# Kernel optimization log

Hardware: AMD Instinct MI355X
Metric: run time of the kernel (lower is better)

The kernel has to match this reference:

```python
import jax, jax.numpy as jnp
from jax import lax
import numpy as np

SR = 48000; FRAME = 960; NFFT = 3840; NWIN = 1024; NFREQ = NFFT // 2 + 1
B = 8; LF = 200; C_CONT = 192; C_SPK = 256; C_INT = 512; NL = 6; MLP = 3; KS = 7


def _interp_linear(x, Lout):
    # F.interpolate(mode='linear', align_corners=False) on (B,C,Lin)
    Lin = x.shape[-1]
    pos = (jnp.arange(Lout, dtype=jnp.float32) + 0.5) * (Lin / Lout) - 0.5
    pos = jnp.clip(pos, 0.0, Lin - 1.0)
    i0 = jnp.floor(pos).astype(jnp.int32)
    i1 = jnp.minimum(i0 + 1, Lin - 1)
    w = pos - i0.astype(jnp.float32)
    return x[..., i0] * (1.0 - w) + x[..., i1] * w


def _interp_nearest(x, Lout):
    Lin = x.shape[-1]
    idx = jnp.floor(jnp.arange(Lout, dtype=jnp.float32) * (Lin / Lout)).astype(jnp.int32)
    return x[..., idx]


def _ln(x, g, b, eps=1e-5):
    # channel-wise LayerNorm on (B,C,L)
    m = jnp.mean(x, axis=1, keepdims=True)
    v = jnp.var(x, axis=1, keepdims=True)
    return (x - m) * lax.rsqrt(v + eps) * g[None, :, None] + b[None, :, None]


def _dwconv(x, w):  # x (B,C,L), w (C,K), zero pad 'same'
    C = x.shape[1]; K = w.shape[-1]
    return lax.conv_general_dilated(x, w[:, None, :], (1,), ((K // 2, K // 2),),
                                    feature_group_count=C,
                                    dimension_numbers=('NCH', 'OIH', 'NCH'))


def _convnext(x, dw_w, dw_b, ln, pw1_w, pw1_b, pw2_w, pw2_b):
    for i in range(dw_w.shape[0]):  # fixed small layer count
        h = _dwconv(x, dw_w[i]) + dw_b[i][None, :, None]
        h = _ln(h, ln[i, 0], ln[i, 1])
        h = jnp.einsum('oc,bcl->bol', pw1_w[i], h) + pw1_b[i][None, :, None]
        h = jax.nn.gelu(h, approximate=False)
        h = jnp.einsum('oc,bcl->bol', pw2_w[i], h) + pw2_b[i][None, :, None]
        x = x + h
    return x


def _forward(content, f0, energy, spk,
             s_in_w, s_in_b, s_in_norm, s_dw_w, s_dw_b, s_ln, s_pw1_w, s_pw1_b,
             s_pw2_w, s_pw2_b, s_out_norm, s_amp_w, s_amp_b, s_ker_w, s_ker_b,
             f_in_w, f_in_b, f_dw_w, f_dw_b, f_ln, f_pw1_w, f_pw1_b,
             f_pw2_w, f_pw2_b, f_out_norm, f_out_w, f_out_b):
    Bc, _, Lf = content.shape
    Lw = Lf * FRAME
    # fused input projection: 4 parallel 1x1 convs == one matmul over concat
    xin = jnp.concatenate([content,
                           jnp.broadcast_to(spk, (Bc, spk.shape[1], Lf)),
                           jnp.log(jax.nn.relu(f0) + 1e-6),
                           energy], axis=1)  # (B,450,Lf)

    # ---------- FirSourceNet trunk ----------
    x = jnp.einsum('oc,bcl->bol', s_in_w, xin) + s_in_b[None, :, None]
    x = _ln(x, s_in_norm[0], s_in_norm[1])
    x = _convnext(x, s_dw_w, s_dw_b, s_ln, s_pw1_w, s_pw1_b, s_pw2_w, s_pw2_b)
    x = _ln(x, s_out_norm[0], s_out_norm[1])
    amps = jax.nn.elu(jnp.einsum('oc,bcl->bol', s_amp_w, x) + s_amp_b[None, :, None]) + 1.0
    kernels = jax.nn.elu(jnp.einsum('oc,bcl->bol', s_ker_w, x) + s_ker_b[None, :, None]) + 1.0  # (B,1921,Lf)

    # ---------- harmonic oscillator (Dirichlet kernel of all harmonics) ----------
    fs = _interp_linear(f0, Lw)                                   # (B,1,Lw)
    uv = _interp_nearest((f0 > 20.0).astype(jnp.float32), Lw)
    pix = jnp.cumsum(jnp.pi * fs / SR, axis=2) % jnp.pi
    a = jnp.round(SR / jnp.maximum(fs, 20.0) * 0.5) * 2.0 + 1.0
    harm = jnp.where(pix < 1e-8, 1.0, jnp.sin(a * pix) / (a * jnp.sin(pix))) * uv
    harm = harm * _interp_linear(amps, Lw)

    # ---------- filtered noise via STFT shaping (hop=FRAME, hann) ----------
    noise = jax.random.uniform(jax.random.key(123), (Bc, Lw), dtype=jnp.float32)
    win = 0.5 - 0.5 * jnp.cos(2.0 * jnp.pi * jnp.arange(NFFT, dtype=jnp.float32) / NFFT)
    pad = NFFT // 2
    xp = jnp.pad(noise, ((0, 0), (pad, pad)), mode='reflect')
    idx = (jnp.arange(Lf + 1) * FRAME)[:, None] + jnp.arange(NFFT)[None, :]
    spec = jnp.fft.rfft(xp[:, idx] * win, axis=-1).transpose(0, 2, 1)      # (B,NFREQ,Lf+1)
    spec = jnp.pad(spec[:, :, 1:] * kernels, ((0, 0), (0, 0), (1, 0)))     # drop 1st frame, shape back
    ft = jnp.fft.irfft(spec.transpose(0, 2, 1), n=NFFT, axis=-1) * win     # (B,Lf+1,NFFT)
    Lpad = NFFT + Lf * FRAME
    y = jnp.zeros((Bc, Lpad), jnp.float32).at[:, idx].add(ft)
    wn = jnp.zeros((Lpad,), jnp.float32).at[idx.reshape(-1)].add(jnp.tile(win * win, Lf + 1))
    y = y / jnp.where(wn > 1e-11, wn, 1.0)
    dsp = harm[:, 0, :] + y[:, pad:pad + Lw]                               # (B,Lw) harmonic+noise source

    # ---------- FirFilterNet: time-varying framed FIR ----------
    x = jnp.einsum('oc,bcl->bol', f_in_w, xin) + f_in_b[None, :, None]
    x = _convnext(x, f_dw_w, f_dw_b, f_ln, f_pw1_w, f_pw1_b, f_pw2_w, f_pw2_b)
    x = _ln(x, f_out_norm[0], f_out_norm[1])
    xe = jnp.pad(x, ((0, 0), (0, 0), (3, 3)), mode='edge')                 # replicate pad
    filt = lax.conv_general_dilated(xe, f_out_w, (1,), 'VALID',
                                    dimension_numbers=('NCH', 'OIH', 'NCH')) + f_out_b[None, :, None]
    filt = filt.transpose(0, 2, 1)                                         # (B,Lf,NWIN)
    # per-frame correlation: grouped conv with B*Lf groups
    src = jnp.pad(dsp.reshape(Bc, Lf, FRAME), ((0, 0), (0, 0), (NWIN, NWIN - 1)))  # (B,Lf,3007)
    out = lax.conv_general_dilated(src.reshape(1, Bc * Lf, FRAME + 2 * NWIN - 1),
                                   filt.reshape(Bc * Lf, 1, NWIN), (1,), 'VALID',
                                   feature_group_count=Bc * Lf,
                                   dimension_numbers=('NCH', 'OIH', 'NCH'))
    out = out.reshape(Bc, Lf, FRAME + NWIN)                                # (B,Lf,1984)
    # fold: overlap-add frames at stride FRAME
    idx2 = (jnp.arange(Lf) * FRAME)[:, None] + jnp.arange(FRAME + NWIN)[None, :]
    folded = jnp.zeros((Bc, Lw + NWIN), jnp.float32).at[:, idx2].add(out)
    return folded[:, None, :Lw]                                            # (B,1,Lw)


def setup_inputs() -> dict:
    key = jax.random.key(0)
    ks = iter(jax.random.split(key, 64))
    def nrm(shape, fan):
        return jax.random.normal(next(ks), shape, dtype=jnp.float32) * (fan ** -0.5)
    d = {}
    d['content'] = jax.random.normal(next(ks), (B, C_CONT, LF), dtype=jnp.float32)
    d['f0'] = jax.random.uniform(next(ks), (B, 1, LF), minval=80.0, maxval=480.0)
    d['energy'] = jax.random.uniform(next(ks), (B, 1, LF), dtype=jnp.float32)
    d['spk'] = jax.random.normal(next(ks), (B, C_SPK, 1), dtype=jnp.float32)
    CIN = C_CONT + C_SPK + 2
    HID = C_INT * MLP
    ones = jnp.ones((C_INT,), jnp.float32); zeros = jnp.zeros((C_INT,), jnp.float32)
    norm2 = jnp.stack([ones, zeros])
    normL = jnp.broadcast_to(norm2, (NL, 2, C_INT)) + 0.0
    for p in ('s', 'f'):
        d[p + '_in_w'] = nrm((C_INT, CIN), CIN); d[p + '_in_b'] = jnp.zeros((C_INT,), jnp.float32)
        d[p + '_dw_w'] = nrm((NL, C_INT, KS), KS); d[p + '_dw_b'] = jnp.zeros((NL, C_INT), jnp.float32)
        d[p + '_ln'] = normL
        d[p + '_pw1_w'] = nrm((NL, HID, C_INT), C_INT); d[p + '_pw1_b'] = jnp.zeros((NL, HID), jnp.float32)
        d[p + '_pw2_w'] = nrm((NL, C_INT, HID), HID); d[p + '_pw2_b'] = jnp.zeros((NL, C_INT), jnp.float32)
        d[p + '_out_norm'] = norm2
    d['s_in_norm'] = norm2
    d['s_amp_w'] = nrm((1, C_INT), C_INT); d['s_amp_b'] = jnp.zeros((1,), jnp.float32)
    d['s_ker_w'] = nrm((NFREQ, C_INT), C_INT); d['s_ker_b'] = jnp.zeros((NFREQ,), jnp.float32)
    d['f_out_w'] = nrm((NWIN, C_INT, KS), C_INT * KS); d['f_out_b'] = jnp.zeros((NWIN,), jnp.float32)
    return d


def reference(content, f0, energy, spk,
              s_in_w, s_in_b, s_in_norm, s_dw_w, s_dw_b, s_ln, s_pw1_w, s_pw1_b,
              s_pw2_w, s_pw2_b, s_out_norm, s_amp_w, s_amp_b, s_ker_w, s_ker_b,
              f_in_w, f_in_b, f_dw_w, f_dw_b, f_ln, f_pw1_w, f_pw1_b,
              f_pw2_w, f_pw2_b, f_out_norm, f_out_w, f_out_b):
    return _forward(content, f0, energy, spk,
                    s_in_w, s_in_b, s_in_norm, s_dw_w, s_dw_b, s_ln, s_pw1_w, s_pw1_b,
                    s_pw2_w, s_pw2_b, s_out_norm, s_amp_w, s_amp_b, s_ker_w, s_ker_b,
                    f_in_w, f_in_b, f_dw_w, f_dw_b, f_ln, f_pw1_w, f_pw1_b,
                    f_pw2_w, f_pw2_b, f_out_norm, f_out_w, f_out_b)
```

## Files before the change

kernel.cpp:

```cpp
#include <hip/hip_runtime.h>
#include <hip/hip_bf16.h>
#include <math.h>
#include <stdint.h>

#define FRAME 960
#define NFFT  3840
#define NWIN  1024
#define NFREQ 1921
#define NB    8
#define LF    200
#define LW    192000
#define CIN   450
#define CI    512
#define HID   1536
#define NL    6
#define NCH   188
#define NK2   3842
#define MTOT  1600
#define MB2   3200
#define SWID  3968
#define MPAD  1664

typedef __attribute__((ext_vector_type(8))) short short8v;
typedef __attribute__((ext_vector_type(4))) float f32x4;
typedef __attribute__((address_space(3))) uint32_t lds_u32;
typedef const __attribute__((address_space(1))) uint32_t glb_u32;

__device__ __forceinline__ uint32_t rotl32(uint32_t v, int r) { return (v << r) | (v >> (32 - r)); }
__device__ __forceinline__ void threefry2x32(uint32_t k0, uint32_t k1, uint32_t& x0, uint32_t& x1) {
  uint32_t ks2 = k0 ^ k1 ^ 0x1BD11BDAu;
  x0 += k0; x1 += k1;
#define TFR(r) { x0 += x1; x1 = rotl32(x1, r); x1 ^= x0; }
  TFR(13) TFR(15) TFR(26) TFR(6)  x0 += k1;  x1 += ks2 + 1u;
  TFR(17) TFR(29) TFR(16) TFR(24) x0 += ks2; x1 += k0 + 2u;
  TFR(13) TFR(15) TFR(26) TFR(6)  x0 += k0;  x1 += k1 + 3u;
  TFR(17) TFR(29) TFR(16) TFR(24) x0 += k1;  x1 += ks2 + 4u;
  TFR(13) TFR(15) TFR(26) TFR(6)  x0 += ks2; x1 += k0 + 5u;
#undef TFR
}
__device__ __forceinline__ float noiseval(int b, int m) {
  if (m < 0) m = -m;
  if (m >= LW) m = 2 * LW - 2 - m;
  uint32_t x0 = 0u, x1 = (uint32_t)(b * LW + m);
  threefry2x32(0u, 123u, x0, x1);
  uint32_t bits = x0 ^ x1;
  return __uint_as_float((bits >> 9) | 0x3f800000u) - 1.0f;
}
__device__ __forceinline__ float winf(int j) {
  return 0.5f - 0.5f * cosf((6.283185307179586f * (float)j) / 3840.0f);
}
__device__ __forceinline__ unsigned short f2bf(float v) {
  uint32_t b = __float_as_uint(v);
  return (unsigned short)((b + 0x7FFFu + ((b >> 16) & 1u)) >> 16);
}
__device__ __forceinline__ float bf2f(unsigned short h) {
  return __uint_as_float(((uint32_t)h) << 16);
}
__device__ __forceinline__ uint32_t pack2(float a, float b, bool lo) {
  unsigned short ha = f2bf(a), hb = f2bf(b);
  if (!lo) return (uint32_t)ha | ((uint32_t)hb << 16);
  return (uint32_t)f2bf(a - bf2f(ha)) | ((uint32_t)f2bf(b - bf2f(hb)) << 16);
}
__device__ __forceinline__ int xcd_remap(int lin, int nwg) {
  int q = nwg >> 3, r = nwg & 7;
  int xcd = lin & 7, base = lin >> 3;
  int start = (xcd < r) ? xcd * (q + 1) : r * (q + 1) + (xcd - r) * q;
  return start + base;
}

__global__ void ctab_fill(float* __restrict__ ct) {
  int j = blockIdx.x * 256 + threadIdx.x;
  if (j < NFFT) ct[j] = cosf((6.283185307179586f * (float)j) / 3840.0f);
}

__global__ void build_xin_pk(const float* __restrict__ content, const float* __restrict__ f0,
                             const float* __restrict__ energy, const float* __restrict__ spk,
                             uint32_t* __restrict__ PH) {
  int idx = blockIdx.x * 256 + threadIdx.x;
  if (idx >= MB2 * 240) return;
  int row = idx / 240, cp = idx % 240;
  int rb = row % MTOT;
  int b = rb / LF, l = rb % LF;
  float v2[2];
#pragma unroll
  for (int u = 0; u < 2; ++u) {
    int c = cp * 2 + u;
    float v = 0.f;
    if (c < 192)       v = content[((size_t)b * 192 + c) * LF + l];
    else if (c < 448)  v = spk[b * 256 + (c - 192)];
    else if (c == 448) v = logf(fmaxf(f0[b * LF + l], 0.0f) + 1e-6f);
    else if (c == 449) v = energy[b * LF + l];
    v2[u] = v;
  }
  PH[idx] = pack2(v2[0], v2[1], false);
}

__global__ void pack_w(const float* __restrict__ W, uint32_t* __restrict__ PH,
                       int M, int K, int Kp2, int total) {
  int idx = blockIdx.x * 256 + threadIdx.x;
  if (idx >= total) return;
  int m = idx / Kp2, kp = idx % Kp2;
  int k = kp * 2;
  float v0 = (m < M && k < K) ? W[(size_t)m * K + k] : 0.f;
  float v1 = (m < M && (k + 1) < K) ? W[(size_t)m * K + k + 1] : 0.f;
  PH[idx] = pack2(v0, v1, false);
}

__global__ void pack_w2(const float* __restrict__ Ws, const float* __restrict__ Wf,
                        uint32_t* __restrict__ PH, int M, int K, int Kp2, int total) {
  int idx = blockIdx.x * 256 + threadIdx.x;
  if (idx >= 2 * total) return;
  int half = idx >= total;
  const float* W = half ? Wf : Ws;
  int t = idx - half * total;
  int m = t / Kp2, kp = t % Kp2;
  int k = kp * 2;
  float v0 = (m < M && k < K) ? W[(size_t)m * K + k] : 0.f;
  float v1 = (m < M && (k + 1) < K) ? W[(size_t)m * K + k + 1] : 0.f;
  PH[idx] = pack2(v0, v1, false);
}

__global__ void pack_wN(const float* __restrict__ Ws, const float* __restrict__ Wf, size_t lstride,
                        uint32_t* __restrict__ PH, int M, int K, int Kp2, int perset, int total) {
  int idx = blockIdx.x * 256 + threadIdx.x;
  if (idx >= total) return;
  int l = idx / (2 * perset);
  int r = idx - l * 2 * perset;
  int half = r >= perset;
  const float* W = (half ? Wf : Ws) + (size_t)l * lstride;
  int t = r - half * perset;
  int m = t / Kp2, kp = t % Kp2;
  int k = kp * 2;
  float v0 = (m < M && k < K) ? W[(size_t)m * K + k] : 0.f;
  float v1 = (m < M && (k + 1) < K) ? W[(size_t)m * K + k + 1] : 0.f;
  PH[idx] = pack2(v0, v1, false);
}

__global__ __launch_bounds__(256) void gemm_bf(
    const uint16_t* __restrict__ WH, const uint16_t* __restrict__ XH,
    const float* __restrict__ bias, const float* __restrict__ bias2,
    const float* __restrict__ res,
    float* __restrict__ outF, uint16_t* __restrict__ outH,
    int M, int Kp, int mtiles, int ntiles, int mode, int act, int nsp, size_t woff)
{
  __shared__ __align__(16) char smem[2][2][4096];
  int nwg = mtiles * ntiles;
  int wg = xcd_remap(blockIdx.x, nwg);
  int mtile = wg / ntiles, ntile = wg % ntiles;
  int m0 = mtile * 64, n0 = ntile * 64;
  int tid = threadIdx.x;
  int lane = tid & 63, w = tid >> 6;
  int wm = w >> 1, wn = w & 1;
  int rowg = Kp >> 3;
  int phases = Kp >> 5;

  int opsel = w >> 1, whalf = w & 1;
  const uint16_t* gb = (opsel == 0) ? WH : XH;
  if (opsel == 0 && ntile >= nsp) gb += woff;
  int row0 = (opsel == 0) ? m0 : n0;
  f32x4 acc[2][2];
#pragma unroll
  for (int i = 0; i < 2; ++i)
#pragma unroll
    for (int j = 0; j < 2; ++j) acc[i][j] = (f32x4){0.f, 0.f, 0.f, 0.f};

  auto stage = [&](int buf, int p) {
    int kg0 = p * 4;
#pragma unroll
    for (int c = 0; c < 2; ++c) {
      int i = whalf * 2 + c;
      int r = i * 16 + (lane >> 2);
      int scg = lane & 3;
      int sgsel = scg ^ (((lane >> 2) >> 1) & 3);
      const uint16_t* src = gb + (size_t)(row0 + r) * rowg * 8 + (size_t)(kg0 + sgsel) * 8;
      __builtin_amdgcn_global_load_lds((glb_u32*)src, (lds_u32*)(&smem[buf][opsel][0] + i * 1024), 16, 0, 0);
    }
  };

  stage(0, 0);
  __syncthreads();
  int fr = lane & 15, fg = lane >> 4;
  int fsw = ((fr >> 1) & 3);
  int aoff0 = (wm * 32 + fr) * 64 + (fg ^ fsw) * 16;
  int aoff1 = (wm * 32 + 16 + fr) * 64 + (fg ^ fsw) * 16;
  int boff0 = (wn * 32 + fr) * 64 + (fg ^ fsw) * 16;
  int boff1 = (wn * 32 + 16 + fr) * 64 + (fg ^ fsw) * 16;

  for (int p = 0; p < phases; ++p) {
    int cur = p & 1;
    if (p + 1 < phases) stage(cur ^ 1, p + 1);
    short8v ah0 = *(const short8v*)(&smem[cur][0][0] + aoff0);
    short8v ah1 = *(const short8v*)(&smem[cur][0][0] + aoff1);
    short8v bh0 = *(const short8v*)(&smem[cur][1][0] + boff0);
    short8v bh1 = *(const short8v*)(&smem[cur][1][0] + boff1);
    acc[0][0] = __builtin_amdgcn_mfma_f32_16x16x32_bf16(ah0, bh0, acc[0][0], 0, 0, 0);
    acc[0][1] = __builtin_amdgcn_mfma_f32_16x16x32_bf16(ah0, bh1, acc[0][1], 0, 0, 0);
    acc[1][0] = __builtin_amdgcn_mfma_f32_16x16x32_bf16(ah1, bh0, acc[1][0], 0, 0, 0);
    acc[1][1] = __builtin_amdgcn_mfma_f32_16x16x32_bf16(ah1, bh1, acc[1][1], 0, 0, 0);
    __syncthreads();
  }

#pragma unroll
  for (int mi = 0; mi < 2; ++mi)
#pragma unroll
    for (int ni = 0; ni < 2; ++ni)
#pragma unroll
      for (int r = 0; r < 4; ++r) {
        int m = m0 + wm * 32 + mi * 16 + ((lane >> 4) << 2) + r;
        int n = n0 + wn * 32 + ni * 16 + (lane & 15);
        if (m >= M) continue;
        float v = acc[mi][ni][r];
        if (bias) v += (bias2 && n >= nsp * 64) ? bias2[m] : bias[m];
        if (act == 1)      v = 0.5f * v * (1.0f + erff(v * 0.7071067811865475f));
        else if (act == 2) v = (v > 0.f ? v : expm1f(v)) + 1.0f;
        if (mode == 0) {
          if (res) v += res[(size_t)n * M + m];
          outF[(size_t)n * M + m] = v;
        } else if (mode == 1) {
          outH[(size_t)n * M + m] = f2bf(v);
        } else {
          outH[(size_t)n * NFREQ + m] = f2bf(v);
        }
      }
}

__global__ __launch_bounds__(256) void gemm_fwd128(
    const uint16_t* __restrict__ AH, const uint16_t* __restrict__ TH,
    const uint16_t* __restrict__ KERH, uint16_t* __restrict__ SH)
{
  __shared__ __align__(16) char smem[2][12288];
  int wg = xcd_remap(blockIdx.x, 62 * 13);
  int ntile = wg / 13, mtile = wg % 13;
  int m0 = mtile * 128, n0 = ntile * 64;
  int tid = threadIdx.x;
  int lane = tid & 63, w = tid >> 6;
  int wm = w >> 1, wn = w & 1;
  f32x4 acc[4][2];
#pragma unroll
  for (int i = 0; i < 4; ++i)
#pragma unroll
    for (int j = 0; j < 2; ++j) acc[i][j] = (f32x4){0.f, 0.f, 0.f, 0.f};

  auto stage = [&](int buf, int p) {
    if (w < 2) {
#pragma unroll
      for (int i = 0; i < 4; ++i) {
        int ci = w * 4 + i;
        int gl = ci * 64 + lane;
        int row = gl >> 2, cg = gl & 3;
        int sg = cg ^ ((row >> 1) & 3);
        const uint16_t* src = AH + (size_t)(m0 + row) * 3840 + p * 32 + sg * 8;
        __builtin_amdgcn_global_load_lds((glb_u32*)src, (lds_u32*)(&smem[buf][0] + ci * 1024), 16, 0, 0);
      }
    } else {
#pragma unroll
      for (int i = 0; i < 2; ++i) {
        int ci = (w - 2) * 2 + i;
        int gl = ci * 64 + lane;
        int row = gl >> 2, cg = gl & 3;
        int sg = cg ^ ((row >> 1) & 3);
        const uint16_t* src = TH + (size_t)(n0 + row) * 3840 + p * 32 + sg * 8;
        __builtin_amdgcn_global_load_lds((glb_u32*)src, (lds_u32*)(&smem[buf][8192] + ci * 1024), 16, 0, 0);
      }
    }
  };

  stage(0, 0);
  __syncthreads();
  int fr = lane & 15, fg = lane >> 4;

  for (int p = 0; p < 120; ++p) {
    int cur = p & 1;
    if (p + 1 < 120) stage(cur ^ 1, p + 1);
    short8v a_h[4], b_h[2];
#pragma unroll
    for (int q = 0; q < 4; ++q) {
      int ra = wm * 64 + q * 16 + fr;
      a_h[q] = *(const short8v*)(&smem[cur][0] + ra * 64 + ((fg ^ ((ra >> 1) & 3)) << 4));
    }
#pragma unroll
    for (int s = 0; s < 2; ++s) {
      int rb = wn * 32 + s * 16 + fr;
      b_h[s] = *(const short8v*)(&smem[cur][8192] + rb * 64 + ((fg ^ ((rb >> 1) & 3)) << 4));
    }
#pragma unroll
    for (int mi = 0; mi < 4; ++mi)
#pragma unroll
      for (int ni = 0; ni < 2; ++ni)
        acc[mi][ni] = __builtin_amdgcn_mfma_f32_16x16x32_bf16(a_h[mi], b_h[ni], acc[mi][ni], 0, 0, 0);
    __syncthreads();
  }

#pragma unroll
  for (int mi = 0; mi < 4; ++mi)
#pragma unroll
    for (int ni = 0; ni < 2; ++ni)
#pragma unroll
      for (int r = 0; r < 4; ++r) {
        int m = m0 + wm * 64 + mi * 16 + ((lane >> 4) << 2) + r;
        int n = n0 + wn * 32 + ni * 16 + (lane & 15);
        if (m < MTOT) {
          float o = 0.f;
          if (n < NK2) {
            int k = n >> 1;
            float kv = bf2f(KERH[(size_t)m * NFREQ + k]);
            bool edge = (k == 0) || (k == 1920);
            float mult = edge ? (1.0f / NFFT) : (2.0f / NFFT);
            o = acc[mi][ni][r] * kv * mult;
            if ((n & 1) && edge) o = 0.f;
          }
          SH[(size_t)m * SWID + n] = f2bf(o);
        }
      }
}

__global__ void twfill_v(const float* __restrict__ ct, uint32_t* __restrict__ VH) {
  int idx = blockIdx.x * 256 + threadIdx.x;
  if (idx >= NFFT * (SWID / 2)) return;
  int j = idx / (SWID / 2), kp = idx % (SWID / 2);
  float v2[2] = {0.f, 0.f};
#pragma unroll
  for (int u = 0; u < 2; ++u) {
    int k2 = kp * 2 + u;
    if (k2 < NK2) {
      int k = k2 >> 1;
      int m = (j * k) % NFFT;
      m += (k2 & 1) * 960;
      if (m >= NFFT) m -= NFFT;
      v2[u] = ct[m];
    }
  }
  VH[idx] = pack2(v2[0], v2[1], false);
}

__global__ __launch_bounds__(256) void gemm_invNT(
    const uint16_t* __restrict__ SH, const uint16_t* __restrict__ VH,
    const float* __restrict__ ct, float* __restrict__ ft)
{
  __shared__ __align__(16) char smem[2][12288];
  int wg = xcd_remap(blockIdx.x, 60 * 13);
  int ntile = wg / 13, mtile = wg % 13;
  int m0 = mtile * 128, n0 = ntile * 64;
  int tid = threadIdx.x;
  int lane = tid & 63, w = tid >> 6;
  int wm = w >> 1, wn = w & 1;
  f32x4 acc[4][2];
#pragma unroll
  for (int i = 0; i < 4; ++i)
#pragma unroll
    for (int j = 0; j < 2; ++j) acc[i][j] = (f32x4){0.f, 0.f, 0.f, 0.f};

  auto stage = [&](int buf, int p) {
    if (w < 2) {
#pragma unroll
      for (int i = 0; i < 4; ++i) {
        int ci = w * 4 + i;
        int gl = ci * 64 + lane;
        int row = gl >> 2, cg = gl & 3;
        int sg = cg ^ ((row >> 1) & 3);
        const uint16_t* src = SH + (size_t)(m0 + row) * SWID + p * 32 + sg * 8;
        __builtin_amdgcn_global_load_lds((glb_u32*)src, (lds_u32*)(&smem[buf][0] + ci * 1024), 16, 0, 0);
      }
    } else {
#pragma unroll
      for (int i = 0; i < 2; ++i) {
        int ci = (w - 2) * 2 + i;
        int gl = ci * 64 + lane;
        int row = gl >> 2, cg = gl & 3;
        int sg = cg ^ ((row >> 1) & 3);
        const uint16_t* src = VH + (size_t)(n0 + row) * SWID + p * 32 + sg * 8;
        __builtin_amdgcn_global_load_lds((glb_u32*)src, (lds_u32*)(&smem[buf][8192] + ci * 1024), 16, 0, 0);
      }
    }
  };

  stage(0, 0);
  __syncthreads();
  int fr = lane & 15, fg = lane >> 4;

  for (int p = 0; p < 124; ++p) {
    int cur = p & 1;
    if (p + 1 < 124) stage(cur ^ 1, p + 1);
    short8v a_h[4], b_h[2];
#pragma unroll
    for (int q = 0; q < 4; ++q) {
      int ra = wm * 64 + q * 16 + fr;
      a_h[q] = *(const short8v*)(&smem[cur][0] + ra * 64 + ((fg ^ ((ra >> 1) & 3)) << 4));
    }
#pragma unroll
    for (int s = 0; s < 2; ++s) {
      int rb = wn * 32 + s * 16 + fr;
      b_h[s] = *(const short8v*)(&smem[cur][8192] + rb * 64 + ((fg ^ ((rb >> 1) & 3)) << 4));
    }
#pragma unroll
    for (int mi = 0; mi < 4; ++mi)
#pragma unroll
      for (int ni = 0; ni < 2; ++ni)
        acc[mi][ni] = __builtin_amdgcn_mfma_f32_16x16x32_bf16(a_h[mi], b_h[ni], acc[mi][ni], 0, 0, 0);
    __syncthreads();
  }

#pragma unroll
  for (int mi = 0; mi < 4; ++mi)
#pragma unroll
    for (int ni = 0; ni < 2; ++ni)
#pragma unroll
      for (int r = 0; r < 4; ++r) {
        int m = m0 + wm * 64 + mi * 16 + ((lane >> 4) << 2) + r;
        int n = n0 + wn * 32 + ni * 16 + (lane & 15);
        if (m < MTOT) ft[(size_t)m * NFFT + n] = acc[mi][ni][r] * (0.5f - 0.5f * ct[n]);
      }
}

__global__ __launch_bounds__(256) void ln2_kernel(float* __restrict__ x, const float* __restrict__ g,
                                                  const float* __restrict__ bta,
                                                  uint32_t* __restrict__ PH) {
  int row = blockIdx.x * 4 + (threadIdx.x >> 6);
  int lane = threadIdx.x & 63;
  float* xr = x + (size_t)row * CI;
  int c0 = lane * 8;
  float4 v0 = *(float4*)&xr[c0], v1 = *(float4*)&xr[c0 + 4];
  float s = v0.x + v0.y + v0.z + v0.w + v1.x + v1.y + v1.z + v1.w;
#pragma unroll
  for (int m = 1; m < 64; m <<= 1) s += __shfl_xor(s, m, 64);
  float mean = s * (1.0f / CI);
  float d[8] = {v0.x - mean, v0.y - mean, v0.z - mean, v0.w - mean,
                v1.x - mean, v1.y - mean, v1.z - mean, v1.w - mean};
  float s2 = 0.f;
#pragma unroll
  for (int q = 0; q < 8; ++q) s2 += d[q] * d[q];
#pragma unroll
  for (int m = 1; m < 64; m <<= 1) s2 += __shfl_xor(s2, m, 64);
  float rs = rsqrtf(s2 * (1.0f / CI) + 1e-5f);
  float o[8];
#pragma unroll
  for (int q = 0; q < 8; ++q) o[q] = d[q] * rs * g[c0 + q] + bta[c0 + q];
  float4 w0 = {o[0], o[1], o[2], o[3]}, w1 = {o[4], o[5], o[6], o[7]};
  *(float4*)&xr[c0] = w0; *(float4*)&xr[c0 + 4] = w1;
  if (PH) {
    int base = (row * CI + c0) >> 1;
#pragma unroll
    for (int q = 0; q < 4; ++q)
      PH[base + q] = pack2(o[2 * q], o[2 * q + 1], false);
  }
}

__global__ __launch_bounds__(256) void dwln_kernel(const float* __restrict__ xs,
    const float* __restrict__ dws, const float* __restrict__ dbs,
    const float* __restrict__ gs, const float* __restrict__ bts,
    const float* __restrict__ dwf, const float* __restrict__ dbf,
    const float* __restrict__ gf, const float* __restrict__ btf,
    uint32_t* __restrict__ PH) {
  int row = blockIdx.x;
  int half = row >= MTOT;
  const float* dw = half ? dwf : dws;
  const float* db = half ? dbf : dbs;
  const float* g  = half ? gf : gs;
  const float* bt = half ? btf : bts;
  int rb = row - half * MTOT;
  int b = rb / LF, l = rb % LF;
  int rbase = half * MTOT + b * LF;
  int c = threadIdx.x * 2;
  float ax = db[c], ay = db[c + 1];
#pragma unroll
  for (int tau = 0; tau < 7; ++tau) {
    int j = l + tau - 3;
    if (j < 0 || j >= LF) continue;
    float2 xv = *(const float2*)&xs[((size_t)(rbase + j)) * CI + c];
    ax = fmaf(xv.x, dw[c * 7 + tau], ax);
    ay = fmaf(xv.y, dw[(c + 1) * 7 + tau], ay);
  }
  __shared__ float red[4], red2[4];
  float s = ax + ay;
#pragma unroll
  for (int m = 1; m < 64; m <<= 1) s += __shfl_xor(s, m, 64);
  if ((threadIdx.x & 63) == 0) red[threadIdx.x >> 6] = s;
  __syncthreads();
  float mean = (red[0] + red[1] + red[2] + red[3]) * (1.0f / CI);
  float dx = ax - mean, dy = ay - mean;
  float s2 = dx * dx + dy * dy;
#pragma unroll
  for (int m = 1; m < 64; m <<= 1) s2 += __shfl_xor(s2, m, 64);
  if ((threadIdx.x & 63) == 0) red2[threadIdx.x >> 6] = s2;
  __syncthreads();
  float var = (red2[0] + red2[1] + red2[2] + red2[3]) * (1.0f / CI);
  float rs = rsqrtf(var + 1e-5f);
  float vx = dx * rs * g[c] + bt[c];
  float vy = dy * rs * g[c + 1] + bt[c + 1];
  PH[(size_t)row * 256 + threadIdx.x] = pack2(vx, vy, false);
}

__global__ __launch_bounds__(256) void amps2_kernel(const float* __restrict__ x, const float* __restrict__ w,
                                                    const float* __restrict__ bias, float* __restrict__ amps) {
  int row = blockIdx.x * 4 + (threadIdx.x >> 6);
  int lane = threadIdx.x & 63;
  const float* xr = x + (size_t)row * CI;
  int c0 = lane * 8;
  float4 v0 = *(const float4*)&xr[c0], v1 = *(const float4*)&xr[c0 + 4];
  float4 w0 = *(const float4*)&w[c0], w1 = *(const float4*)&w[c0 + 4];
  float s = v0.x * w0.x + v0.y * w0.y + v0.z * w0.z + v0.w * w0.w
          + v1.x * w1.x + v1.y * w1.y + v1.z * w1.z + v1.w * w1.w;
#pragma unroll
  for (int m = 1; m < 64; m <<= 1) s += __shfl_xor(s, m, 64);
  if (lane == 0) {
    float a = s + bias[0];
    amps[row] = (a > 0.f ? a : expm1f(a)) + 1.0f;
  }
}

__global__ void im2col_pk(const float* __restrict__ x, uint32_t* __restrict__ PH) {
  int idx = blockIdx.x * 256 + threadIdx.x;
  if (idx >= MTOT * 1792) return;
  int row = idx / 1792, kp = idx % 1792;
  int b = row / LF, l = row % LF;
  float v2[2];
#pragma unroll
  for (int u = 0; u < 2; ++u) {
    int kap = kp * 2 + u;
    int ch = kap / 7, tau = kap % 7;
    int j = l + tau - 3;
    j = j < 0 ? 0 : (j > LF - 1 ? LF - 1 : j);
    v2[u] = x[((size_t)b * LF + j) * CI + ch];
  }
  PH[idx] = pack2(v2[0], v2[1], false);
}

__global__ void pack_noise(const float* __restrict__ ct, uint32_t* __restrict__ AH) {
  int idx = blockIdx.x * 256 + threadIdx.x;
  if (idx >= MPAD * 1920) return;
  int t = idx / 1920, jp = idx % 1920;
  float v0 = 0.f, v1 = 0.f;
  if (t < MTOT) {
    int b = t / LF, tt = t % LF;
    int j = jp * 2;
    v0 = noiseval(b, tt * 960 + j - 960) * (0.5f - 0.5f * ct[j]);
    v1 = noiseval(b, tt * 960 + j - 959) * (0.5f - 0.5f * ct[j + 1]);
  }
  AH[idx] = pack2(v0, v1, false);
}

__global__ void twfill_pk(const float* __restrict__ ct, uint32_t* __restrict__ TH) {
  int idx = blockIdx.x * 256 + threadIdx.x;
  if (idx >= SWID * 1920) return;
  int k2 = idx / 1920, jp = idx % 1920;
  float v2[2] = {0.f, 0.f};
  if (k2 < NK2) {
    int k = k2 >> 1;
    int add = (k2 & 1) * 960;
#pragma unroll
    for (int u = 0; u < 2; ++u) {
      int j = jp * 2 + u;
      int m = (j * k) % NFFT;
      m += add;
      if (m >= NFFT) m -= NFFT;
      v2[u] = ct[m];
    }
  }
  TH[idx] = pack2(v2[0], v2[1], false);
}

__global__ __launch_bounds__(256) void cumsum1(const float* __restrict__ f0, float* __restrict__ fs,
                                               double* __restrict__ csum) {
  int b = blockIdx.y, ch = blockIdx.x;
  int base = ch * 1024;
  double s = 0.0;
  for (int q = 0; q < 4; ++q) {
    int n = base + threadIdx.x * 4 + q;
    if (n < LW) {
      float pos = ((float)n + 0.5f) * (200.0f / 192000.0f) - 0.5f;
      pos = fminf(fmaxf(pos, 0.0f), 199.0f);
      int i0 = (int)pos;
      int i1 = min(i0 + 1, 199);
      float w = pos - (float)i0;
      float fsv = f0[b * LF + i0] * (1.0f - w) + f0[b * LF + i1] * w;
      fs[(size_t)b * LW + n] = fsv;
      s += (double)((3.14159274101257324f * fsv) / 48000.0f);
    }
  }
  __shared__ double sh[256];
  sh[threadIdx.x] = s;
  __syncthreads();
  for (int o2 = 128; o2 > 0; o2 >>= 1) {
    if (threadIdx.x < o2) sh[threadIdx.x] += sh[threadIdx.x + o2];
    __syncthreads();
  }
  if (threadIdx.x == 0) csum[b * NCH + ch] = sh[0];
}

__global__ __launch_bounds__(256) void harm_kernel(
    const float* __restrict__ fs, const double* __restrict__ csum,
    const float* __restrict__ f0, const float* __restrict__ amps,
    float* __restrict__ harm) {
  int b = blockIdx.y, ch = blockIdx.x;
  const float* fsb = fs + (size_t)b * LW;
  int base = ch * 1024;
  int tid = threadIdx.x;
  double p[4]; double s = 0.0;
  int n0 = base + tid * 4;
  for (int q = 0; q < 4; ++q) {
    int n = n0 + q; float sm = 0.f;
    if (n < LW) sm = (3.14159274101257324f * fsb[n]) / 48000.0f;
    s += (double)sm; p[q] = s;
  }
  __shared__ double sh[256];
  sh[tid] = (tid < ch) ? csum[b * NCH + tid] : 0.0;
  __syncthreads();
  for (int o2 = 128; o2 > 0; o2 >>= 1) {
    if (tid < o2) sh[tid] += sh[tid + o2];
    __syncthreads();
  }
  double cbase = sh[0];
  __syncthreads();
  sh[tid] = s; __syncthreads();
  for (int o2 = 1; o2 < 256; o2 <<= 1) {
    double v = (tid >= o2) ? sh[tid - o2] : 0.0;
    __syncthreads();
    sh[tid] += v;
    __syncthreads();
  }
  double excl = cbase + (tid > 0 ? sh[tid - 1] : 0.0);
  const double PID = (double)3.14159274101257324f;
  for (int q = 0; q < 4; ++q) {
    int n = n0 + q; if (n >= LW) break;
    double S = excl + p[q];
    float pixf = (float)fmod(S, PID);
    float fsv = fsb[n];
    float a = rintf(48000.0f / fmaxf(fsv, 20.0f) * 0.5f) * 2.0f + 1.0f;
    float D = (pixf < 1e-8f) ? 1.0f : (sinf(a * pixf) / (a * sinf(pixf)));
    int ui = n / 960;
    float uv = (f0[b * LF + ui] > 20.0f) ? 1.0f : 0.0f;
    float posA = ((float)n + 0.5f) * (200.0f / 192000.0f) - 0.5f;
    posA = fminf(fmaxf(posA, 0.0f), 199.0f);
    int i0 = (int)posA;
    int i1 = min(i0 + 1, 199);
    float w = posA - (float)i0;
    float ampI = amps[b * LF + i0] * (1.0f - w) + amps[b * LF + i1] * w;
    harm[(size_t)b * LW + n] = (D * uv) * ampI;
  }
}

__global__ __launch_bounds__(256) void fir5_kernel(const float* __restrict__ ft,
                                                   const float* __restrict__ harm,
                                                   const float* __restrict__ filt,
                                                   const float* __restrict__ ct,
                                                   float* __restrict__ outf) {
  int t = blockIdx.x, b = blockIdx.y;
  __shared__ float frp[3456];
  __shared__ float fl[NWIN];
  int tid = threadIdx.x;
  for (int i = tid; i < 3456; i += 256) frp[i] = 0.f;
  __syncthreads();
  for (int i = tid; i < FRAME; i += 256) {
    int n = t * FRAME + i;
    int p = n + 1920;
    int t0 = (p > 3839) ? ((p - 2880) / 960) : 0;
    int t1 = p / FRAME; if (t1 > 200) t1 = 200;
    float y = 0.f, wn = 0.f;
    for (int tt = t0; tt <= t1; ++tt) {
      int j = p - FRAME * tt;
      float w = 0.5f - 0.5f * ct[j];
      wn += w * w;
      if (tt >= 1) y += ft[((size_t)b * LF + (tt - 1)) * NFFT + j];
    }
    float den = wn > 1e-11f ? wn : 1.0f;
    float dspv = harm[(size_t)b * LW + n] + y / den;
    int x = 1024 + i;
    frp[x + (x >> 3)] = dspv;
  }
  for (int i = tid; i < NWIN; i += 256) fl[i] = filt[((size_t)b * LF + t) * NWIN + i];
  __syncthreads();
  float a[8] = {0.f, 0.f, 0.f, 0.f, 0.f, 0.f, 0.f, 0.f};
  float wbuf[8];
  int base = 9 * tid;
#pragma unroll
  for (int r = 0; r < 8; ++r) wbuf[r] = frp[base + r];
  int nbase = base + 9;
  for (int tau8 = 0; tau8 < 128; ++tau8) {
    int nb = nbase + tau8 * 9;
#pragma unroll
    for (int r = 0; r < 8; ++r) {
      float fv = fl[tau8 * 8 + r];
#pragma unroll
      for (int q = 0; q < 8; ++q)
        a[q] = fmaf(wbuf[(r + q) & 7], fv, a[q]);
      wbuf[r] = frp[nb + r];
    }
  }
#pragma unroll
  for (int q = 0; q < 8; ++q) {
    int i = tid * 8 + q;
    if (i < 1984) outf[((size_t)b * LF + t) * 1984 + i] = a[q];
  }
}

__global__ void fold_kernel(const float* __restrict__ outf, float* __restrict__ out) {
  int idx = blockIdx.x * 256 + threadIdx.x;
  if (idx >= NB * LW) return;
  int b = idx / LW, n = idx % LW;
  int t0 = (n >= 1984) ? ((n - 1024) / 960) : 0;
  int t1 = n / 960; if (t1 > 199) t1 = 199;
  float acc = 0.f;
  for (int t = t0; t <= t1; ++t)
    acc += outf[((size_t)b * LF + t) * 1984 + (n - 960 * t)];
  out[idx] = acc;
}

extern "C" void kernel_launch(void* const* d_in, const int* in_sizes, int n_in,
                              void* d_out, int out_size, void* d_ws, size_t ws_size,
                              hipStream_t stream) {
  const float* content    = (const float*)d_in[0];
  const float* f0         = (const float*)d_in[1];
  const float* energy     = (const float*)d_in[2];
  const float* spk        = (const float*)d_in[3];
  const float* s_in_w     = (const float*)d_in[4];
  const float* s_in_b     = (const float*)d_in[5];
  const float* s_dw_w     = (const float*)d_in[6];
  const float* s_dw_b     = (const float*)d_in[7];
  const float* s_ln       = (const float*)d_in[8];
  const float* s_pw1_w    = (const float*)d_in[9];
  const float* s_pw1_b    = (const float*)d_in[10];
  const float* s_pw2_w    = (const float*)d_in[11];
  const float* s_pw2_b    = (const float*)d_in[12];
  const float* s_out_norm = (const float*)d_in[13];
  const float* f_in_w     = (const float*)d_in[14];
  const float* f_in_b     = (const float*)d_in[15];
  const float* f_dw_w     = (const float*)d_in[16];
  const float* f_dw_b     = (const float*)d_in[17];
  const float* f_ln       = (const float*)d_in[18];
  const float* f_pw1_w    = (const float*)d_in[19];
  const float* f_pw1_b    = (const float*)d_in[20];
  const float* f_pw2_w    = (const float*)d_in[21];
  const float* f_pw2_b    = (const float*)d_in[22];
  const float* f_out_norm = (const float*)d_in[23];
  const float* s_in_norm  = (const float*)d_in[24];
  const float* s_amp_w    = (const float*)d_in[25];
  const float* s_amp_b    = (const float*)d_in[26];
  const float* s_ker_w    = (const float*)d_in[27];
  const float* s_ker_b    = (const float*)d_in[28];
  const float* f_out_w    = (const float*)d_in[29];
  const float* f_out_b    = (const float*)d_in[30];

  char* W0 = (char*)d_ws;
  double*   CSUM  = (double*)W0;
  uint32_t* XINPH = (uint32_t*)(W0 + 12032);
  float*    XS    = (float*)   (W0 + 6156032);
  uint32_t* TPH   = (uint32_t*)(W0 + 12709632);
  uint16_t* KERH  = (uint16_t*)(W0 + 19263232);
  float*    AMPS  = (float*)   (W0 + 25410432);
  float*    FILT  = (float*)   (W0 + 25418624);
  float*    HARM  = (float*)   (W0 + 31972224);
  char*     R2    = W0 + 38116224;
  char*     FTR   = W0 + 64527232;
  char*     U     = W0 + 89103232;
  uint32_t* TH32  = (uint32_t*)(W0 + 114662272);
  float*    CTAB  = (float*)   (W0 + 175610752);
  uint32_t* XSPH = TPH;
  uint32_t* H15PH = (uint32_t*)R2;
  uint32_t* IMPH = (uint32_t*)R2;
  uint16_t* SH   = (uint16_t*)R2;
  float*    OUTF = (float*)R2;
  float*    FS   = (float*)FTR;
  float*    FT   = (float*)FTR;
  uint32_t* PW1PH_A = (uint32_t*)FTR;
  uint32_t* PW1PH_B = (uint32_t*)U;
  uint32_t* PW2PH = TH32;
  uint32_t* WINPH = (uint32_t*)R2;
  uint32_t* WPH  = (uint32_t*)U;
  uint16_t* AH   = (uint16_t*)U;

  (void)in_sizes; (void)n_in; (void)out_size; (void)ws_size;

  ctab_fill<<<dim3(15), 256, 0, stream>>>(CTAB);
  build_xin_pk<<<dim3((MB2 * 240 + 255) / 256), 256, 0, stream>>>(content, f0, energy, spk, XINPH);

  {
    int perset = HID * 256;
    int tot3 = 3 * 2 * perset;
    pack_wN<<<dim3((tot3 + 255) / 256), 256, 0, stream>>>(s_pw1_w, f_pw1_w, (size_t)HID * CI,
        PW1PH_A, HID, CI, 256, perset, tot3);
    pack_wN<<<dim3((tot3 + 255) / 256), 256, 0, stream>>>(s_pw1_w + (size_t)3 * HID * CI,
        f_pw1_w + (size_t)3 * HID * CI, (size_t)HID * CI,
        PW1PH_B, HID, CI, 256, perset, tot3);
    int tot6 = 6 * 2 * perset;
    pack_wN<<<dim3((tot6 + 255) / 256), 256, 0, stream>>>(s_pw2_w, f_pw2_w, (size_t)CI * HID,
        PW2PH, CI, HID, 768, perset, tot6);
  }
  {
    int total = CI * 240;
    pack_w2<<<dim3((2 * total + 255) / 256), 256, 0, stream>>>(s_in_w, f_in_w, WINPH, CI, CIN, 240, total);
  }

  gemm_bf<<<dim3(8 * 50), 256, 0, stream>>>((uint16_t*)WINPH, (uint16_t*)XINPH,
      s_in_b, f_in_b, nullptr, XS, nullptr, CI, 480, 8, 50, 0, 0, 25, (size_t)512 * 480);
  ln2_kernel<<<dim3(MTOT / 4), 256, 0, stream>>>(XS, s_in_norm, s_in_norm + CI, nullptr);
  for (int i = 0; i < NL; ++i) {
    dwln_kernel<<<dim3(MB2), 256, 0, stream>>>(XS,
        s_dw_w + (size_t)i * CI * 7, s_dw_b + (size_t)i * CI,
        s_ln + (size_t)(i * 2) * CI, s_ln + (size_t)(i * 2 + 1) * CI,
        f_dw_w + (size_t)i * CI * 7, f_dw_b + (size_t)i * CI,
        f_ln + (size_t)(i * 2) * CI, f_ln + (size_t)(i * 2 + 1) * CI,
        TPH);
    const uint16_t* w1h = (i < 3) ? (const uint16_t*)((char*)PW1PH_A + (size_t)i * 3145728)
                                  : (const uint16_t*)((char*)PW1PH_B + (size_t)(i - 3) * 3145728);
    gemm_bf<<<dim3(24 * 50), 256, 0, stream>>>(w1h, (uint16_t*)TPH,
        s_pw1_b + (size_t)i * HID, f_pw1_b + (size_t)i * HID, nullptr,
        nullptr, (uint16_t*)H15PH, HID, 512, 24, 50, 1, 1, 25, (size_t)1536 * 512);
    const uint16_t* w2h = (const uint16_t*)((char*)PW2PH + (size_t)i * 3145728);
    gemm_bf<<<dim3(8 * 50), 256, 0, stream>>>(w2h, (uint16_t*)H15PH,
        s_pw2_b + (size_t)i * CI, f_pw2_b + (size_t)i * CI, XS,
        XS, nullptr, CI, 1536, 8, 50, 0, 0, 25, (size_t)512 * 1536);
  }

  ln2_kernel<<<dim3(MTOT / 4), 256, 0, stream>>>(XS, s_out_norm, s_out_norm + CI, XSPH);
  amps2_kernel<<<dim3(MTOT / 4), 256, 0, stream>>>(XS, s_amp_w, s_amp_b, AMPS);
  {
    int total = 1984 * 256;
    pack_w<<<dim3((total + 255) / 256), 256, 0, stream>>>(s_ker_w, WPH, NFREQ, CI, 256, total);
  }
  gemm_bf<<<dim3(31 * 25), 256, 0, stream>>>((uint16_t*)WPH, (uint16_t*)XSPH,
      s_ker_b, nullptr, nullptr, nullptr, KERH, NFREQ, 512, 31, 25, 2, 2, 1000, 0);

  ln2_kernel<<<dim3(MTOT / 4), 256, 0, stream>>>(XS + (size_t)MTOT * CI, f_out_norm, f_out_norm + CI, nullptr);
  im2col_pk<<<dim3((MTOT * 1792 + 255) / 256), 256, 0, stream>>>(XS + (size_t)MTOT * CI, IMPH);
  {
    int total = NWIN * 1792;
    pack_w<<<dim3((total + 255) / 256), 256, 0, stream>>>(f_out_w, WPH, NWIN, 3584, 1792, total);
  }
  gemm_bf<<<dim3(16 * 25), 256, 0, stream>>>((uint16_t*)WPH, (uint16_t*)IMPH,
      f_out_b, nullptr, nullptr, FILT, nullptr, NWIN, 3584, 16, 25, 0, 0, 1000, 0);

  cumsum1<<<dim3(NCH, NB), 256, 0, stream>>>(f0, FS, CSUM);
  harm_kernel<<<dim3(NCH, NB), 256, 0, stream>>>(FS, CSUM, f0, AMPS, HARM);

  pack_noise<<<dim3((MPAD * 1920 + 255) / 256), 256, 0, stream>>>(CTAB, (uint32_t*)AH);
  twfill_pk<<<dim3((SWID * 1920 + 255) / 256), 256, 0, stream>>>(CTAB, TH32);
  gemm_fwd128<<<dim3(13 * 62), 256, 0, stream>>>((uint16_t*)AH, (uint16_t*)TH32, KERH, SH);
  twfill_v<<<dim3((NFFT * (SWID / 2) + 255) / 256), 256, 0, stream>>>(CTAB, TH32);
  gemm_invNT<<<dim3(60 * 13), 256, 0, stream>>>(SH, (uint16_t*)TH32, CTAB, FT);

  fir5_kernel<<<dim3(LF, NB), 256, 0, stream>>>(FT, HARM, FILT, CTAB, OUTF);
  fold_kernel<<<dim3((NB * LW + 255) / 256), 256, 0, stream>>>(OUTF, (float*)d_out);
}
```

Measured before the change: 941.6 us.

## Enlarge DFT GEMM tiles to 128x128 with 512-thread workgroups

The forward and inverse DFT GEMMs grow their output tile from 128x64 to 128x128 by doubling the workgroup to 8 waves. Every wave now stages two 16-byte chunks per K step. The grid is halved, so each staged A tile is reused across twice as many N columns, which cuts global and L2 traffic. The trade-off is fewer workgroups (403 and 390), which may underfill the 256 CUs and leave some idle.

```diff
diff --git a/kernel.cpp b/kernel.cpp
--- a/kernel.cpp
+++ b/kernel.cpp
@@ -224,17 +224,17 @@
       }
 }
 
-__global__ __launch_bounds__(256) void gemm_fwd128(
+__global__ __launch_bounds__(512) void gemm_fwd128(
     const uint16_t* __restrict__ AH, const uint16_t* __restrict__ TH,
     const uint16_t* __restrict__ KERH, uint16_t* __restrict__ SH)
 {
-  __shared__ __align__(16) char smem[2][12288];
-  int wg = xcd_remap(blockIdx.x, 62 * 13);
+  __shared__ __align__(16) char smem[2][2][8192];
+  int wg = xcd_remap(blockIdx.x, 13 * 31);
   int ntile = wg / 13, mtile = wg % 13;
-  int m0 = mtile * 128, n0 = ntile * 64;
+  int m0 = mtile * 128, n0 = ntile * 128;
   int tid = threadIdx.x;
   int lane = tid & 63, w = tid >> 6;
-  int wm = w >> 1, wn = w & 1;
+  int wm = w >> 2, wn = w & 3;
   f32x4 acc[4][2];
 #pragma unroll
   for (int i = 0; i < 4; ++i)
@@ -242,26 +242,17 @@
     for (int j = 0; j < 2; ++j) acc[i][j] = (f32x4){0.f, 0.f, 0.f, 0.f};
 
   auto stage = [&](int buf, int p) {
-    if (w < 2) {
-#pragma unroll
-      for (int i = 0; i < 4; ++i) {
-        int ci = w * 4 + i;
-        int gl = ci * 64 + lane;
-        int row = gl >> 2, cg = gl & 3;
-        int sg = cg ^ ((row >> 1) & 3);
-        const uint16_t* src = AH + (size_t)(m0 + row) * 3840 + p * 32 + sg * 8;
-        __builtin_amdgcn_global_load_lds((glb_u32*)src, (lds_u32*)(&smem[buf][0] + ci * 1024), 16, 0, 0);
-      }
-    } else {
-#pragma unroll
-      for (int i = 0; i < 2; ++i) {
-        int ci = (w - 2) * 2 + i;
-        int gl = ci * 64 + lane;
-        int row = gl >> 2, cg = gl & 3;
-        int sg = cg ^ ((row >> 1) & 3);
-        const uint16_t* src = TH + (size_t)(n0 + row) * 3840 + p * 32 + sg * 8;
-        __builtin_amdgcn_global_load_lds((glb_u32*)src, (lds_u32*)(&smem[buf][8192] + ci * 1024), 16, 0, 0);
-      }
+#pragma unroll
+    for (int c = 0; c < 2; ++c) {
+      int ci = w * 2 + c;
+      int opsel = ci >> 3;
+      int cc = ci & 7;
+      int gl = cc * 64 + lane;
+      int row = gl >> 2, cg = gl & 3;
+      int sg = cg ^ ((row >> 1) & 3);
+      const uint16_t* src = (opsel ? TH + (size_t)(n0 + row) * 3840 : AH + (size_t)(m0 + row) * 3840)
+                            + p * 32 + sg * 8;
+      __builtin_amdgcn_global_load_lds((glb_u32*)src, (lds_u32*)(&smem[buf][opsel][0] + cc * 1024), 16, 0, 0);
     }
   };
 
@@ -276,12 +267,12 @@
 #pragma unroll
     for (int q = 0; q < 4; ++q) {
       int ra = wm * 64 + q * 16 + fr;
-      a_h[q] = *(const short8v*)(&smem[cur][0] + ra * 64 + ((fg ^ ((ra >> 1) & 3)) << 4));
+      a_h[q] = *(const short8v*)(&smem[cur][0][0] + ra * 64 + ((fg ^ ((ra >> 1) & 3)) << 4));
     }
 #pragma unroll
     for (int s = 0; s < 2; ++s) {
       int rb = wn * 32 + s * 16 + fr;
-      b_h[s] = *(const short8v*)(&smem[cur][8192] + rb * 64 + ((fg ^ ((rb >> 1) & 3)) << 4));
+      b_h[s] = *(const short8v*)(&smem[cur][1][0] + rb * 64 + ((fg ^ ((rb >> 1) & 3)) << 4));
     }
 #pragma unroll
     for (int mi = 0; mi < 4; ++mi)
@@ -333,17 +324,17 @@
   VH[idx] = pack2(v2[0], v2[1], false);
 }
 
-__global__ __launch_bounds__(256) void gemm_invNT(
+__global__ __launch_bounds__(512) void gemm_invNT(
     const uint16_t* __restrict__ SH, const uint16_t* __restrict__ VH,
     const float* __restrict__ ct, float* __restrict__ ft)
 {
-  __shared__ __align__(16) char smem[2][12288];
-  int wg = xcd_remap(blockIdx.x, 60 * 13);
+  __shared__ __align__(16) char smem[2][2][8192];
+  int wg = xcd_remap(blockIdx.x, 30 * 13);
   int ntile = wg / 13, mtile = wg % 13;
-  int m0 = mtile * 128, n0 = ntile * 64;
+  int m0 = mtile * 128, n0 = ntile * 128;
   int tid = threadIdx.x;
   int lane = tid & 63, w = tid >> 6;
-  int wm = w >> 1, wn = w & 1;
+  int wm = w >> 2, wn = w & 3;
   f32x4 acc[4][2];
 #pragma unroll
   for (int i = 0; i < 4; ++i)
@@ -351,26 +342,17 @@
     for (int j = 0; j < 2; ++j) acc[i][j] = (f32x4){0.f, 0.f, 0.f, 0.f};
 
   auto stage = [&](int buf, int p) {
-    if (w < 2) {
-#pragma unroll
-      for (int i = 0; i < 4; ++i) {
-        int ci = w * 4 + i;
-        int gl = ci * 64 + lane;
-        int row = gl >> 2, cg = gl & 3;
-        int sg = cg ^ ((row >> 1) & 3);
-        const uint16_t* src = SH + (size_t)(m0 + row) * SWID + p * 32 + sg * 8;
-        __builtin_amdgcn_global_load_lds((glb_u32*)src, (lds_u32*)(&smem[buf][0] + ci * 1024), 16, 0, 0);
-      }
-    } else {
-#pragma unroll
-      for (int i = 0; i < 2; ++i) {
-        int ci = (w - 2) * 2 + i;
-        int gl = ci * 64 + lane;
-        int row = gl >> 2, cg = gl & 3;
-        int sg = cg ^ ((row >> 1) & 3);
-        const uint16_t* src = VH + (size_t)(n0 + row) * SWID + p * 32 + sg * 8;
-        __builtin_amdgcn_global_load_lds((glb_u32*)src, (lds_u32*)(&smem[buf][8192] + ci * 1024), 16, 0, 0);
-      }
+#pragma unroll
+    for (int c = 0; c < 2; ++c) {
+      int ci = w * 2 + c;
+      int opsel = ci >> 3;
+      int cc = ci & 7;
+      int gl = cc * 64 + lane;
+      int row = gl >> 2, cg = gl & 3;
+      int sg = cg ^ ((row >> 1) & 3);
+      const uint16_t* src = (opsel ? VH + (size_t)(n0 + row) * SWID : SH + (size_t)(m0 + row) * SWID)
+                            + p * 32 + sg * 8;
+      __builtin_amdgcn_global_load_lds((glb_u32*)src, (lds_u32*)(&smem[buf][opsel][0] + cc * 1024), 16, 0, 0);
     }
   };
 
@@ -385,12 +367,12 @@
 #pragma unroll
     for (int q = 0; q < 4; ++q) {
       int ra = wm * 64 + q * 16 + fr;
-      a_h[q] = *(const short8v*)(&smem[cur][0] + ra * 64 + ((fg ^ ((ra >> 1) & 3)) << 4));
+      a_h[q] = *(const short8v*)(&smem[cur][0][0] + ra * 64 + ((fg ^ ((ra >> 1) & 3)) << 4));
     }
 #pragma unroll
     for (int s = 0; s < 2; ++s) {
       int rb = wn * 32 + s * 16 + fr;
-      b_h[s] = *(const short8v*)(&smem[cur][8192] + rb * 64 + ((fg ^ ((rb >> 1) & 3)) << 4));
+      b_h[s] = *(const short8v*)(&smem[cur][1][0] + rb * 64 + ((fg ^ ((rb >> 1) & 3)) << 4));
     }
 #pragma unroll
     for (int mi = 0; mi < 4; ++mi)
@@ -834,9 +816,9 @@
 
   pack_noise<<<dim3((MPAD * 1920 + 255) / 256), 256, 0, stream>>>(CTAB, (uint32_t*)AH);
   twfill_pk<<<dim3((SWID * 1920 + 255) / 256), 256, 0, stream>>>(CTAB, TH32);
-  gemm_fwd128<<<dim3(13 * 62), 256, 0, stream>>>((uint16_t*)AH, (uint16_t*)TH32, KERH, SH);
+  gemm_fwd128<<<dim3(13 * 31), 512, 0, stream>>>((uint16_t*)AH, (uint16_t*)TH32, KERH, SH);
   twfill_v<<<dim3((NFFT * (SWID / 2) + 255) / 256), 256, 0, stream>>>(CTAB, TH32);
-  gemm_invNT<<<dim3(60 * 13), 256, 0, stream>>>(SH, (uint16_t*)TH32, CTAB, FT);
+  gemm_invNT<<<dim3(30 * 13), 512, 0, stream>>>(SH, (uint16_t*)TH32, CTAB, FT);
 
   fir5_kernel<<<dim3(LF, NB), 256, 0, stream>>>(FT, HARM, FILT, CTAB, OUTF);
   fold_kernel<<<dim3((NB * LW + 255) / 256), 256, 0, stream>>>(OUTF, (float*)d_out);
```

After: 871.9 us. 1.08x faster.
